# Optimization experiments

Hardware: AMD Instinct MI355X
Metric: run time of the kernel (lower is better)

## Reference

```python
import jax, jax.numpy as jnp
import numpy as np

N = 4096      # tokens
D = 4096      # input_dim
O = 4096      # output_dim
E = 8         # n_experts
R = 16        # LoRA rank (same for all experts)
K = 2         # top_k
TEMP = 1.0    # temperature
ALPHA = 1.0   # LoRA alpha


def setup_inputs() -> dict:
    key = jax.random.key(0)
    ks = jax.random.split(key, 7)
    std = 1.0 / np.sqrt(R)  # LoRALayer init: randn(input_dim, rank) * 1/sqrt(rank)
    return {
        "x": jax.random.normal(ks[0], (N, D), jnp.float32),
        "linear_w": jax.random.normal(ks[1], (D, O), jnp.float32) * 0.02,  # base nn.Linear weight (stored [in,out])
        "linear_b": jnp.zeros((O,), jnp.float32),
        "lora_A": jax.random.normal(ks[2], (E, D, R), jnp.float32) * std,
        "lora_B": jax.random.normal(ks[3], (E, R, O), jnp.float32) * 0.02,  # torch inits B to 0; randomized for nontrivial test
        "gate_w": jax.random.normal(ks[4], (E + 1, D), jnp.float32) * 0.02,  # E+1 GateLayers, each [D,1]
        "bvv": jax.random.randint(ks[5], (N, E), 0, 2, jnp.int32),  # basis_variant_binary_vector (unused in static gating)
    }


def reference(x, linear_w, linear_b, lora_A, lora_B, gate_w, bvv):
    # base path: nn.Linear
    base = x @ linear_w + linear_b                                   # [N, O]
    # all experts evaluated densely: alpha * (x @ A_e @ B_e), batched as grouped GEMMs
    lora = ALPHA * jnp.einsum("ner,ero->neo",
                              jnp.einsum("nd,edr->ner", x, lora_A),
                              lora_B)                                # [N, E, O]
    outputs = jnp.concatenate([base[:, None, :], lora], axis=1)      # [N, E+1, O]

    # static top-k gating
    logits = x @ gate_w.T                                            # [N, E+1]
    base_logits, lora_logits = logits[:, :1], logits[:, 1:]
    top_vals, top_idx = jax.lax.top_k(lora_logits, K)                # [N, K]
    rows = jnp.arange(x.shape[0])[:, None]
    # torch: zeros.scatter(top_idx, top_vals) -> non-selected experts keep logit 0.0
    lora_sparse = jnp.zeros_like(lora_logits).at[rows, top_idx].set(top_vals)
    gates = jax.nn.softmax(
        jnp.concatenate([base_logits, lora_sparse], axis=-1) / TEMP, axis=-1
    )                                                                # [N, E+1]

    return jnp.sum(outputs * gates[..., None], axis=1)               # [N, O]
```

## Files before the change

### kernel.cpp

```cpp
#include <hip/hip_runtime.h>
#include <hip/hip_bf16.h>
#include <math.h>

constexpr int Ncfg = 4096;
constexpr int Dcfg = 4096;
constexpr int Ocfg = 4096;
constexpr int Ecfg = 8;
constexpr int Rcfg = 16;
constexpr int KD   = Dcfg + Ecfg * Rcfg;
constexpr int NKT  = KD / 64;
constexpr float ALPHA_C = 1.0f;
constexpr double TEMP_C = 1.0;

constexpr size_t BT_OFF = 0;
constexpr size_t AP_OFF = BT_OFF + (size_t)Ocfg * KD * 2;
constexpr size_t AT_OFF = AP_OFF + (size_t)Ncfg * KD * 2;
constexpr size_t G_OFF  = AT_OFF + (size_t)Ecfg * Rcfg * Dcfg * 2;

typedef short bf16x8 __attribute__((ext_vector_type(8)));
typedef float f32x4  __attribute__((ext_vector_type(4)));

__device__ __forceinline__ void async_load16(const __hip_bfloat16* g, __hip_bfloat16* l) {
  __builtin_amdgcn_global_load_lds((__attribute__((address_space(1))) void*)(g),
                                   (__attribute__((address_space(3))) void*)(l), 16, 0, 0);
}

__global__ __launch_bounds__(256) void prep_parallel_kernel(
    const float* __restrict__ x,  const float* __restrict__ gw,
    const float* __restrict__ W,  const float* __restrict__ lB,
    const float* __restrict__ lA,
    float* __restrict__ gates, __hip_bfloat16* __restrict__ Ap,
    __hip_bfloat16* __restrict__ BT, __hip_bfloat16* __restrict__ AT) {
  __shared__ union {
    float tile[64][65];
    float atile[256][17];
  } sm;
  const int bid = blockIdx.x;
  const int tid = threadIdx.x;

  if (bid < 512) {
    const int wave = tid >> 6, lane = tid & 63;
    const int na = bid * 8 + wave * 2, nb = na + 1;
    const float4* xa4 = (const float4*)(x + (size_t)na * Dcfg);
    const float4* xb4 = (const float4*)(x + (size_t)nb * Dcfg);
    const float4* gw4 = (const float4*)gw;
    double accA[9], accB[9];
#pragma unroll
    for (int e = 0; e < 9; e++) { accA[e] = 0.0; accB[e] = 0.0; }
    for (int i = 0; i < 16; i++) {
      int fi = lane + 64 * i;
      float4 xa = xa4[fi], xb = xb4[fi];
#pragma unroll
      for (int e = 0; e < 9; e++) {
        float4 w = gw4[e * 1024 + fi];
        accA[e] += (double)xa.x * (double)w.x + (double)xa.y * (double)w.y +
                   (double)xa.z * (double)w.z + (double)xa.w * (double)w.w;
        accB[e] += (double)xb.x * (double)w.x + (double)xb.y * (double)w.y +
                   (double)xb.z * (double)w.z + (double)xb.w * (double)w.w;
      }
    }
#pragma unroll
    for (int off = 32; off >= 1; off >>= 1) {
#pragma unroll
      for (int e = 0; e < 9; e++) {
        accA[e] += __shfl_xor(accA[e], off, 64);
        accB[e] += __shfl_xor(accB[e], off, 64);
      }
    }
    float g0A_l = 0.f, g0B_l = 0.f;
    if (lane == 0) {
#pragma unroll
      for (int r = 0; r < 2; r++) {
        double lg[9];
#pragma unroll
        for (int e = 0; e < 9; e++) lg[e] = r ? accB[e] : accA[e];
        int i1 = 1;
        for (int e = 2; e <= 8; e++) if (lg[e] > lg[i1]) i1 = e;
        int i2 = -1; double v2 = -1e300;
        for (int e = 1; e <= 8; e++) if (e != i1 && lg[e] > v2) { v2 = lg[e]; i2 = e; }
        double vals[9];
        vals[0] = lg[0];
        for (int e = 1; e <= 8; e++) vals[e] = (e == i1 || e == i2) ? lg[e] : 0.0;
        double mx = vals[0];
        for (int e = 1; e < 9; e++) mx = fmax(mx, vals[e]);
        double se = 0.0, ex[9];
        for (int e = 0; e < 9; e++) { ex[e] = exp((vals[e] - mx) / TEMP_C); se += ex[e]; }
        const int n = r ? nb : na;
        for (int e = 0; e < 9; e++) gates[n * 16 + e] = (float)(ex[e] / se);
        if (r == 0) g0A_l = (float)(ex[0] / se); else g0B_l = (float)(ex[0] / se);
      }
    }
    const float g0A = __shfl(g0A_l, 0, 64);
    const float g0B = __shfl(g0B_l, 0, 64);
    __hip_bfloat16* ara = Ap + (size_t)na * KD;
    __hip_bfloat16* arb = Ap + (size_t)nb * KD;
    for (int i = 0; i < 16; i++) {
      int fi = lane + 64 * i;
      float4 xa = xa4[fi], xb = xb4[fi];
      union { ushort4 u; __hip_bfloat16 h[4]; } p;
      p.h[0] = __float2bfloat16(g0A * xa.x);
      p.h[1] = __float2bfloat16(g0A * xa.y);
      p.h[2] = __float2bfloat16(g0A * xa.z);
      p.h[3] = __float2bfloat16(g0A * xa.w);
      *(ushort4*)(ara + (size_t)fi * 4) = p.u;
      p.h[0] = __float2bfloat16(g0B * xb.x);
      p.h[1] = __float2bfloat16(g0B * xb.y);
      p.h[2] = __float2bfloat16(g0B * xb.z);
      p.h[3] = __float2bfloat16(g0B * xb.w);
      *(ushort4*)(arb + (size_t)fi * 4) = p.u;
    }
  } else if (bid < 4736) {
    const float* src; int r0, c0, dstOff;
    if (bid < 4608) {
      int id = bid - 512;
      src = W; r0 = (id & 63) * 64; c0 = (id >> 6) * 64; dstOff = 0;
    } else {
      int id = bid - 4608;
      src = lB; r0 = (id & 1) * 64; c0 = (id >> 1) * 64; dstOff = Dcfg;
    }
#pragma unroll
    for (int it = 0; it < 4; it++) {
      int flat = it * 256 + tid;
      int i = flat >> 4, f = flat & 15;
      float4 v = *(const float4*)(src + (size_t)(r0 + i) * Ocfg + c0 + 4 * f);
      sm.tile[i][4 * f + 0] = v.x;
      sm.tile[i][4 * f + 1] = v.y;
      sm.tile[i][4 * f + 2] = v.z;
      sm.tile[i][4 * f + 3] = v.w;
    }
    __syncthreads();
#pragma unroll
    for (int it = 0; it < 4; it++) {
      int flat = it * 256 + tid;
      int j = flat >> 4, q = flat & 15;
      union { ushort4 u; __hip_bfloat16 h[4]; } p;
      p.h[0] = __float2bfloat16(sm.tile[4 * q + 0][j]);
      p.h[1] = __float2bfloat16(sm.tile[4 * q + 1][j]);
      p.h[2] = __float2bfloat16(sm.tile[4 * q + 2][j]);
      p.h[3] = __float2bfloat16(sm.tile[4 * q + 3][j]);
      *(ushort4*)(BT + (size_t)(c0 + j) * KD + dstOff + r0 + 4 * q) = p.u;
    }
  } else {
    const int id = bid - 4736;
    const int e = id >> 4, d0 = (id & 15) * 256;
#pragma unroll
    for (int it = 0; it < 16; it++) {
      int idx = it * 256 + tid;
      int d = idx >> 4, rr = idx & 15;
      sm.atile[d][rr] = lA[((size_t)e * Dcfg + d0 + d) * Rcfg + rr];
    }
    __syncthreads();
#pragma unroll
    for (int rr = 0; rr < Rcfg; rr++) {
      AT[((size_t)e * Rcfg + rr) * Dcfg + d0 + tid] = __float2bfloat16(sm.atile[tid][rr]);
    }
  }
}

__global__ __launch_bounds__(512) void lora_t_kernel(
    const float* __restrict__ x, const __hip_bfloat16* __restrict__ AT,
    const float* __restrict__ gates, __hip_bfloat16* __restrict__ Ap) {
  const int n0 = blockIdx.x * 16;
  const int tid = threadIdx.x;
  const int wave = tid >> 6, lane = tid & 63;
  const int m = lane & 15, quad = lane >> 4;
  const int kbase = wave * 512;

  f32x4 acc[8] = {};
  const float* xrow = x + (size_t)(n0 + m) * Dcfg + kbase + quad * 8;
  const __hip_bfloat16* atb = AT + (size_t)m * Dcfg + kbase + quad * 8;
#pragma unroll 2
  for (int kb = 0; kb < 512; kb += 32) {
    float4 x0 = *(const float4*)(xrow + kb);
    float4 x1 = *(const float4*)(xrow + kb + 4);
    union { bf16x8 v; __hip_bfloat16 h[8]; } a;
    a.h[0] = __float2bfloat16(x0.x); a.h[1] = __float2bfloat16(x0.y);
    a.h[2] = __float2bfloat16(x0.z); a.h[3] = __float2bfloat16(x0.w);
    a.h[4] = __float2bfloat16(x1.x); a.h[5] = __float2bfloat16(x1.y);
    a.h[6] = __float2bfloat16(x1.z); a.h[7] = __float2bfloat16(x1.w);
#pragma unroll
    for (int e = 0; e < Ecfg; e++) {
      bf16x8 b = *(const bf16x8*)(atb + (size_t)e * Rcfg * Dcfg + kb);
      acc[e] = __builtin_amdgcn_mfma_f32_16x16x32_bf16(a.v, b, acc[e], 0, 0, 0);
    }
  }
  __shared__ f32x4 red[8][8][64];
#pragma unroll
  for (int e = 0; e < Ecfg; e++) red[wave][e][lane] = acc[e];
  __syncthreads();
  {
    const int e = wave;
    f32x4 s = red[0][e][lane];
#pragma unroll
    for (int w = 1; w < 8; w++) s += red[w][e][lane];
#pragma unroll
    for (int rg = 0; rg < 4; rg++) {
      int nn = n0 + quad * 4 + rg;
      float g = gates[nn * 16 + 1 + e];
      Ap[(size_t)nn * KD + Dcfg + e * Rcfg + m] = __float2bfloat16(ALPHA_C * g * s[rg]);
    }
  }
}

#define STG(gbase, lbase, u, ktile)                                              \
  __builtin_amdgcn_global_load_lds(                                              \
      (__attribute__((address_space(1))) void*)((gbase) + (size_t)(u) * 64 * KD  \
                                                + (size_t)(ktile) * 64),         \
      (__attribute__((address_space(3))) void*)((lbase) + (u) * 8192 + dst),     \
      16, 0, 0)

__global__ __launch_bounds__(512, 2) void gemm_kernel(
    const __hip_bfloat16* __restrict__ Ap, const __hip_bfloat16* __restrict__ BT,
    const float* __restrict__ gates, const float* __restrict__ bias,
    float* __restrict__ out) {
  __shared__ char smem[131072];
  const int tid = threadIdx.x;
  const int m0 = blockIdx.y * 256, n0 = blockIdx.x * 256;
  const int wave = tid >> 6, lane = tid & 63;
  const int wm = wave >> 2, wn = wave & 3;
  const int mr = lane & 15, quad = lane >> 4;

  const int trow = tid >> 3;
  const int cswz = (((tid & 7) ^ ((tid >> 3) & 7)) << 3);
  const __hip_bfloat16* gA = Ap + (size_t)(m0 + trow) * KD + cswz;
  const __hip_bfloat16* gB = BT + (size_t)(n0 + trow) * KD + cswz;
  const int dst = tid << 4;

  const int rswz = (mr & 7) << 4;
  const int arow = (wm * 128 + mr) * 128;
  const int brow = (wn * 64 + mr) * 128;

  f32x4 acc[8][4] = {};

  STG(gA, smem,          0, 0); STG(gA, smem,          1, 0);
  STG(gA, smem,          2, 0); STG(gA, smem,          3, 0);
  STG(gB, smem + 32768,  0, 0); STG(gB, smem + 32768,  1, 0);
  STG(gB, smem + 32768,  2, 0); STG(gB, smem + 32768,  3, 0);
  STG(gA, smem + 65536,  0, 1); STG(gA, smem + 65536,  1, 1);
  STG(gA, smem + 65536,  2, 1); STG(gA, smem + 65536,  3, 1);
  STG(gB, smem + 98304,  0, 1); STG(gB, smem + 98304,  1, 1);
  asm volatile("s_waitcnt vmcnt(6)" ::: "memory");
  __builtin_amdgcn_s_barrier();

  for (int kt = 0; kt < NKT; ++kt) {
    const bool odd = kt & 1;
    const char* At = odd ? (smem + 65536) : smem;
    const char* Bt = odd ? (smem + 98304) : (smem + 32768);
    char* Bn = odd ? (smem + 32768) : (smem + 98304);

    bf16x8 b[4][2], aX[2][2], aY[2][2];

#pragma unroll
    for (int j = 0; j < 4; ++j)
#pragma unroll
      for (int kh = 0; kh < 2; ++kh)
        b[j][kh] = *(const bf16x8*)(Bt + brow + j * 2048 + ((kh * 64 + quad * 16) ^ rswz));
#pragma unroll
    for (int i = 0; i < 2; ++i)
#pragma unroll
      for (int kh = 0; kh < 2; ++kh)
        aX[i][kh] = *(const bf16x8*)(At + arow + i * 2048 + ((kh * 64 + quad * 16) ^ rswz));
    if (kt + 1 < NKT) { STG(gB, Bn, 2, kt + 1); STG(gB, Bn, 3, kt + 1); }
#pragma unroll
    for (int i = 0; i < 2; ++i)
#pragma unroll
      for (int kh = 0; kh < 2; ++kh)
        aY[i][kh] = *(const bf16x8*)(At + arow + (2 + i) * 2048 + ((kh * 64 + quad * 16) ^ rswz));

    __builtin_amdgcn_s_setprio(1);
#pragma unroll
    for (int i = 0; i < 2; ++i)
#pragma unroll
      for (int j = 0; j < 4; ++j)
#pragma unroll
        for (int kh = 0; kh < 2; ++kh)
          acc[i][j] = __builtin_amdgcn_mfma_f32_16x16x32_bf16(aX[i][kh], b[j][kh], acc[i][j], 0, 0, 0);
    __builtin_amdgcn_s_setprio(0);
#pragma unroll
    for (int i = 0; i < 2; ++i)
#pragma unroll
      for (int kh = 0; kh < 2; ++kh)
        aX[i][kh] = *(const bf16x8*)(At + arow + (4 + i) * 2048 + ((kh * 64 + quad * 16) ^ rswz));

    __builtin_amdgcn_s_setprio(1);
#pragma unroll
    for (int i = 0; i < 2; ++i)
#pragma unroll
      for (int j = 0; j < 4; ++j)
#pragma unroll
        for (int kh = 0; kh < 2; ++kh)
          acc[2 + i][j] = __builtin_amdgcn_mfma_f32_16x16x32_bf16(aY[i][kh], b[j][kh], acc[2 + i][j], 0, 0, 0);
    __builtin_amdgcn_s_setprio(0);
#pragma unroll
    for (int i = 0; i < 2; ++i)
#pragma unroll
      for (int kh = 0; kh < 2; ++kh)
        aY[i][kh] = *(const bf16x8*)(At + arow + (6 + i) * 2048 + ((kh * 64 + quad * 16) ^ rswz));

    __builtin_amdgcn_s_setprio(1);
#pragma unroll
    for (int i = 0; i < 2; ++i)
#pragma unroll
      for (int j = 0; j < 4; ++j)
#pragma unroll
        for (int kh = 0; kh < 2; ++kh)
          acc[4 + i][j] = __builtin_amdgcn_mfma_f32_16x16x32_bf16(aX[i][kh], b[j][kh], acc[4 + i][j], 0, 0, 0);
    __builtin_amdgcn_s_setprio(0);

    asm volatile("s_waitcnt lgkmcnt(0)" ::: "memory");
    __builtin_amdgcn_sched_barrier(0);
    __builtin_amdgcn_s_barrier();

    if (kt + 2 < NKT) {
      char* Ac = (char*)At; char* Bc = (char*)Bt;
      STG(gA, Ac, 0, kt + 2); STG(gA, Ac, 1, kt + 2);
      STG(gA, Ac, 2, kt + 2); STG(gA, Ac, 3, kt + 2);
      STG(gB, Bc, 0, kt + 2); STG(gB, Bc, 1, kt + 2);
    }
    __builtin_amdgcn_s_setprio(1);
#pragma unroll
    for (int i = 0; i < 2; ++i)
#pragma unroll
      for (int j = 0; j < 4; ++j)
#pragma unroll
        for (int kh = 0; kh < 2; ++kh)
          acc[6 + i][j] = __builtin_amdgcn_mfma_f32_16x16x32_bf16(aY[i][kh], b[j][kh], acc[6 + i][j], 0, 0, 0);
    __builtin_amdgcn_s_setprio(0);
    if (kt + 2 < NKT) {
      asm volatile("s_waitcnt vmcnt(6)" ::: "memory");
    } else if (kt + 1 < NKT) {
      asm volatile("s_waitcnt vmcnt(0)" ::: "memory");
    }
    if (kt + 1 < NKT) __builtin_amdgcn_s_barrier();
  }

  float bv[4];
#pragma unroll
  for (int j = 0; j < 4; ++j) bv[j] = bias[n0 + wn * 64 + j * 16 + mr];
#pragma unroll
  for (int i = 0; i < 8; ++i) {
    const int rowb = m0 + wm * 128 + i * 16 + quad * 4;
#pragma unroll
    for (int rg = 0; rg < 4; ++rg) {
      const int row = rowb + rg;
      const float g0 = gates[row * 16];
      float* orow = out + (size_t)row * Ocfg + n0 + wn * 64 + mr;
#pragma unroll
      for (int j = 0; j < 4; ++j)
        orow[j * 16] = acc[i][j][rg] + g0 * bv[j];
    }
  }
}

extern "C" void kernel_launch(void* const* d_in, const int* in_sizes, int n_in,
                              void* d_out, int out_size, void* d_ws, size_t ws_size,
                              hipStream_t stream) {
  const float* x  = (const float*)d_in[0];
  const float* W  = (const float*)d_in[1];
  const float* b  = (const float*)d_in[2];
  const float* lA = (const float*)d_in[3];
  const float* lB = (const float*)d_in[4];
  const float* gw = (const float*)d_in[5];
  float* out = (float*)d_out;

  char* ws = (char*)d_ws;
  __hip_bfloat16* BT    = (__hip_bfloat16*)(ws + BT_OFF);
  __hip_bfloat16* Ap    = (__hip_bfloat16*)(ws + AP_OFF);
  __hip_bfloat16* AT    = (__hip_bfloat16*)(ws + AT_OFF);
  float*          gates = (float*)(ws + G_OFF);

  prep_parallel_kernel<<<dim3(4864), 256, 0, stream>>>(x, gw, W, lB, lA, gates, Ap, BT, AT);
  lora_t_kernel<<<dim3(Ncfg / 16), 512, 0, stream>>>(x, AT, gates, Ap);
  gemm_kernel<<<dim3(Ocfg / 256, Ncfg / 256), 512, 0, stream>>>(Ap, BT, gates, b, out);
}
```

Baseline: 348.4 us.

## Move weight transposition into LoRA projection kernel to overlap prep stages

Regroups the preprocessing kernels so the first kernel computes only the gates, the scaled x rows and the AT transpose. A second kernel then runs the LoRA down-projection blocks alongside the W and lora_B transpose/convert blocks. This lets the large W transpose run concurrently with the small LoRA projection instead of in a separate earlier launch. The transpose blocks now use 512 threads with fewer iterations each, and the shared memory is unioned between the transpose tile and the reduction buffer.

```diff
diff --git a/kernel.cpp b/kernel.cpp
--- a/kernel.cpp
+++ b/kernel.cpp
@@ -20,21 +20,12 @@
 typedef short bf16x8 __attribute__((ext_vector_type(8)));
 typedef float f32x4  __attribute__((ext_vector_type(4)));
 
-__device__ __forceinline__ void async_load16(const __hip_bfloat16* g, __hip_bfloat16* l) {
-  __builtin_amdgcn_global_load_lds((__attribute__((address_space(1))) void*)(g),
-                                   (__attribute__((address_space(3))) void*)(l), 16, 0, 0);
-}
-
-__global__ __launch_bounds__(256) void prep_parallel_kernel(
+__global__ __launch_bounds__(256) void gates_at_kernel(
     const float* __restrict__ x,  const float* __restrict__ gw,
-    const float* __restrict__ W,  const float* __restrict__ lB,
     const float* __restrict__ lA,
     float* __restrict__ gates, __hip_bfloat16* __restrict__ Ap,
-    __hip_bfloat16* __restrict__ BT, __hip_bfloat16* __restrict__ AT) {
-  __shared__ union {
-    float tile[64][65];
-    float atile[256][17];
-  } sm;
+    __hip_bfloat16* __restrict__ AT) {
+  __shared__ float atile[256][17];
   const int bid = blockIdx.x;
   const int tid = threadIdx.x;
 
@@ -109,18 +100,86 @@
       p.h[3] = __float2bfloat16(g0B * xb.w);
       *(ushort4*)(arb + (size_t)fi * 4) = p.u;
     }
-  } else if (bid < 4736) {
+  } else {
+    const int id = bid - 512;
+    const int e = id >> 4, d0 = (id & 15) * 256;
+#pragma unroll
+    for (int it = 0; it < 16; it++) {
+      int idx = it * 256 + tid;
+      int d = idx >> 4, rr = idx & 15;
+      atile[d][rr] = lA[((size_t)e * Dcfg + d0 + d) * Rcfg + rr];
+    }
+    __syncthreads();
+#pragma unroll
+    for (int rr = 0; rr < Rcfg; rr++) {
+      AT[((size_t)e * Rcfg + rr) * Dcfg + d0 + tid] = __float2bfloat16(atile[tid][rr]);
+    }
+  }
+}
+
+__global__ __launch_bounds__(512) void trans_lora_kernel(
+    const float* __restrict__ x,  const float* __restrict__ W,
+    const float* __restrict__ lB, const __hip_bfloat16* __restrict__ AT,
+    const float* __restrict__ gates,
+    __hip_bfloat16* __restrict__ Ap, __hip_bfloat16* __restrict__ BT) {
+  __shared__ union {
+    float tile[64][65];
+    f32x4 red[8][8][64];
+  } sm;
+  const int bid = blockIdx.x;
+  const int tid = threadIdx.x;
+
+  if (bid < 256) {
+    const int n0 = bid * 16;
+    const int wave = tid >> 6, lane = tid & 63;
+    const int m = lane & 15, quad = lane >> 4;
+    const int kbase = wave * 512;
+
+    f32x4 acc[8] = {};
+    const float* xrow = x + (size_t)(n0 + m) * Dcfg + kbase + quad * 8;
+    const __hip_bfloat16* atb = AT + (size_t)m * Dcfg + kbase + quad * 8;
+#pragma unroll 2
+    for (int kb = 0; kb < 512; kb += 32) {
+      float4 x0 = *(const float4*)(xrow + kb);
+      float4 x1 = *(const float4*)(xrow + kb + 4);
+      union { bf16x8 v; __hip_bfloat16 h[8]; } a;
+      a.h[0] = __float2bfloat16(x0.x); a.h[1] = __float2bfloat16(x0.y);
+      a.h[2] = __float2bfloat16(x0.z); a.h[3] = __float2bfloat16(x0.w);
+      a.h[4] = __float2bfloat16(x1.x); a.h[5] = __float2bfloat16(x1.y);
+      a.h[6] = __float2bfloat16(x1.z); a.h[7] = __float2bfloat16(x1.w);
+#pragma unroll
+      for (int e = 0; e < Ecfg; e++) {
+        bf16x8 b = *(const bf16x8*)(atb + (size_t)e * Rcfg * Dcfg + kb);
+        acc[e] = __builtin_amdgcn_mfma_f32_16x16x32_bf16(a.v, b, acc[e], 0, 0, 0);
+      }
+    }
+#pragma unroll
+    for (int e = 0; e < Ecfg; e++) sm.red[wave][e][lane] = acc[e];
+    __syncthreads();
+    {
+      const int e = wave;
+      f32x4 s = sm.red[0][e][lane];
+#pragma unroll
+      for (int w = 1; w < 8; w++) s += sm.red[w][e][lane];
+#pragma unroll
+      for (int rg = 0; rg < 4; rg++) {
+        int nn = n0 + quad * 4 + rg;
+        float g = gates[nn * 16 + 1 + e];
+        Ap[(size_t)nn * KD + Dcfg + e * Rcfg + m] = __float2bfloat16(ALPHA_C * g * s[rg]);
+      }
+    }
+  } else {
     const float* src; int r0, c0, dstOff;
-    if (bid < 4608) {
-      int id = bid - 512;
+    if (bid < 4352) {
+      int id = bid - 256;
       src = W; r0 = (id & 63) * 64; c0 = (id >> 6) * 64; dstOff = 0;
     } else {
-      int id = bid - 4608;
+      int id = bid - 4352;
       src = lB; r0 = (id & 1) * 64; c0 = (id >> 1) * 64; dstOff = Dcfg;
     }
 #pragma unroll
-    for (int it = 0; it < 4; it++) {
-      int flat = it * 256 + tid;
+    for (int it = 0; it < 2; it++) {
+      int flat = it * 512 + tid;
       int i = flat >> 4, f = flat & 15;
       float4 v = *(const float4*)(src + (size_t)(r0 + i) * Ocfg + c0 + 4 * f);
       sm.tile[i][4 * f + 0] = v.x;
@@ -130,8 +189,8 @@
     }
     __syncthreads();
 #pragma unroll
-    for (int it = 0; it < 4; it++) {
-      int flat = it * 256 + tid;
+    for (int it = 0; it < 2; it++) {
+      int flat = it * 512 + tid;
       int j = flat >> 4, q = flat & 15;
       union { ushort4 u; __hip_bfloat16 h[4]; } p;
       p.h[0] = __float2bfloat16(sm.tile[4 * q + 0][j]);
@@ -139,65 +198,6 @@
       p.h[2] = __float2bfloat16(sm.tile[4 * q + 2][j]);
       p.h[3] = __float2bfloat16(sm.tile[4 * q + 3][j]);
       *(ushort4*)(BT + (size_t)(c0 + j) * KD + dstOff + r0 + 4 * q) = p.u;
-    }
-  } else {
-    const int id = bid - 4736;
-    const int e = id >> 4, d0 = (id & 15) * 256;
-#pragma unroll
-    for (int it = 0; it < 16; it++) {
-      int idx = it * 256 + tid;
-      int d = idx >> 4, rr = idx & 15;
-      sm.atile[d][rr] = lA[((size_t)e * Dcfg + d0 + d) * Rcfg + rr];
-    }
-    __syncthreads();
-#pragma unroll
-    for (int rr = 0; rr < Rcfg; rr++) {
-      AT[((size_t)e * Rcfg + rr) * Dcfg + d0 + tid] = __float2bfloat16(sm.atile[tid][rr]);
-    }
-  }
-}
-
-__global__ __launch_bounds__(512) void lora_t_kernel(
-    const float* __restrict__ x, const __hip_bfloat16* __restrict__ AT,
-    const float* __restrict__ gates, __hip_bfloat16* __restrict__ Ap) {
-  const int n0 = blockIdx.x * 16;
-  const int tid = threadIdx.x;
-  const int wave = tid >> 6, lane = tid & 63;
-  const int m = lane & 15, quad = lane >> 4;
-  const int kbase = wave * 512;
-
-  f32x4 acc[8] = {};
-  const float* xrow = x + (size_t)(n0 + m) * Dcfg + kbase + quad * 8;
-  const __hip_bfloat16* atb = AT + (size_t)m * Dcfg + kbase + quad * 8;
-#pragma unroll 2
-  for (int kb = 0; kb < 512; kb += 32) {
-    float4 x0 = *(const float4*)(xrow + kb);
-    float4 x1 = *(const float4*)(xrow + kb + 4);
-    union { bf16x8 v; __hip_bfloat16 h[8]; } a;
-    a.h[0] = __float2bfloat16(x0.x); a.h[1] = __float2bfloat16(x0.y);
-    a.h[2] = __float2bfloat16(x0.z); a.h[3] = __float2bfloat16(x0.w);
-    a.h[4] = __float2bfloat16(x1.x); a.h[5] = __float2bfloat16(x1.y);
-    a.h[6] = __float2bfloat16(x1.z); a.h[7] = __float2bfloat16(x1.w);
-#pragma unroll
-    for (int e = 0; e < Ecfg; e++) {
-      bf16x8 b = *(const bf16x8*)(atb + (size_t)e * Rcfg * Dcfg + kb);
-      acc[e] = __builtin_amdgcn_mfma_f32_16x16x32_bf16(a.v, b, acc[e], 0, 0, 0);
-    }
-  }
-  __shared__ f32x4 red[8][8][64];
-#pragma unroll
-  for (int e = 0; e < Ecfg; e++) red[wave][e][lane] = acc[e];
-  __syncthreads();
-  {
-    const int e = wave;
-    f32x4 s = red[0][e][lane];
-#pragma unroll
-    for (int w = 1; w < 8; w++) s += red[w][e][lane];
-#pragma unroll
-    for (int rg = 0; rg < 4; rg++) {
-      int nn = n0 + quad * 4 + rg;
-      float g = gates[nn * 16 + 1 + e];
-      Ap[(size_t)nn * KD + Dcfg + e * Rcfg + m] = __float2bfloat16(ALPHA_C * g * s[rg]);
     }
   }
 }
@@ -369,7 +369,7 @@
   __hip_bfloat16* AT    = (__hip_bfloat16*)(ws + AT_OFF);
   float*          gates = (float*)(ws + G_OFF);
 
-  prep_parallel_kernel<<<dim3(4864), 256, 0, stream>>>(x, gw, W, lB, lA, gates, Ap, BT, AT);
-  lora_t_kernel<<<dim3(Ncfg / 16), 512, 0, stream>>>(x, AT, gates, Ap);
+  gates_at_kernel<<<dim3(640), 256, 0, stream>>>(x, gw, lA, gates, Ap, AT);
+  trans_lora_kernel<<<dim3(4480), 512, 0, stream>>>(x, W, lB, AT, gates, Ap, BT);
   gemm_kernel<<<dim3(Ocfg / 256, Ncfg / 256), 512, 0, stream>>>(Ap, BT, gates, b, out);
 }
```

Measured after the change: 344.6 us. About the same (-1.1%).
